# Kernel optimization log

Measured on AMD Instinct MI355X. Metric: run time of the kernel, lower is better.

## Reference

```python
import jax, jax.numpy as jnp
import numpy as np
import math

B, S, DIM = 2, 2048, 4096
N_HEADS, N_KV = 32, 8
HD = DIM // N_HEADS           # 128
N_REP = N_HEADS // N_KV       # 4
MAX_SEQ = 2048


def _rope_freqs(seq_len, head_dim):
    inv = 1.0 / (10000.0 ** (np.arange(0, head_dim, 2, dtype=np.float32) / head_dim))
    ang = np.outer(np.arange(seq_len, dtype=np.float32), inv)  # [S, HD/2]
    return jnp.asarray(np.cos(ang)), jnp.asarray(np.sin(ang))


def setup_inputs() -> dict:
    key = jax.random.key(0)
    ks = jax.random.split(key, 5)
    x = jax.random.normal(ks[0], (B, S, DIM), dtype=jnp.float32)
    wq = jax.random.normal(ks[1], (DIM, N_HEADS * HD), dtype=jnp.float32) * 0.02
    wk = jax.random.normal(ks[2], (DIM, N_KV * HD), dtype=jnp.float32) * 0.02
    wv = jax.random.normal(ks[3], (DIM, N_KV * HD), dtype=jnp.float32) * 0.02
    wo = jax.random.normal(ks[4], (N_HEADS * HD, DIM), dtype=jnp.float32) * 0.02
    freqs_cos, freqs_sin = _rope_freqs(S, HD)
    return {"x": x, "wq": wq, "wk": wk, "wv": wv, "wo": wo,
            "freqs_cos": freqs_cos, "freqs_sin": freqs_sin, "start_pos": 0}


def _apply_rope(t, cos, sin):
    # t: [B, S, H, HD]; adjacent pairs (2i, 2i+1) form complex numbers
    tr = t.reshape(*t.shape[:-1], HD // 2, 2)
    xr, xi = tr[..., 0], tr[..., 1]
    c = cos[None, :, None, :]  # [1, S, 1, HD/2]
    s = sin[None, :, None, :]
    o = jnp.stack([xr * c - xi * s, xr * s + xi * c], axis=-1)
    return o.reshape(t.shape)


def reference(x, wq, wk, wv, wo, freqs_cos, freqs_sin, start_pos):
    batch, seq_len, _ = x.shape
    q = (x @ wq).reshape(batch, seq_len, N_HEADS, HD)
    k = (x @ wk).reshape(batch, seq_len, N_KV, HD)
    v = (x @ wv).reshape(batch, seq_len, N_KV, HD)
    xq = _apply_rope(q, freqs_cos, freqs_sin)
    xk = _apply_rope(k, freqs_cos, freqs_sin)

    # KV-cache append (buffer initialized to zeros, as in the module)
    cache_k = jnp.zeros((batch, MAX_SEQ, N_KV, HD), dtype=x.dtype)
    cache_v = jnp.zeros((batch, MAX_SEQ, N_KV, HD), dtype=x.dtype)
    cache_k = jax.lax.dynamic_update_slice(cache_k, xk, (0, start_pos, 0, 0))
    cache_v = jax.lax.dynamic_update_slice(cache_v, v, (0, start_pos, 0, 0))
    keys = cache_k[:, : start_pos + seq_len]    # [B, T, KV, HD]
    values = cache_v[:, : start_pos + seq_len]

    # GQA: repeat kv heads n_rep times
    keys = jnp.repeat(keys, N_REP, axis=2)      # [B, T, H, HD]
    values = jnp.repeat(values, N_REP, axis=2)

    # [B, H, Sq, T] scores; no causal mask, matching the original module
    scores = jnp.einsum("bqhd,bkhd->bhqk", xq, keys) / math.sqrt(HD)
    attn = jax.nn.softmax(scores, axis=-1)
    out = jnp.einsum("bhqk,bkhd->bqhd", attn, values)
    out = out.reshape(batch, seq_len, N_HEADS * HD)
    return out @ wo
```

## Files before the change

kernel.cpp:

```cpp
#include <hip/hip_runtime.h>

#define S_LEN 2048

typedef __bf16 bf16x8 __attribute__((ext_vector_type(8)));
typedef float f32x4 __attribute__((ext_vector_type(4)));

static __device__ __forceinline__ unsigned short f32_to_bf16(float f){
  unsigned int u = __float_as_uint(f);
  u += 0x7FFFu + ((u >> 16) & 1u);
  return (unsigned short)(u >> 16);
}
static __device__ __forceinline__ float bf16_to_f32(unsigned short h){
  return __uint_as_float(((unsigned int)h) << 16);
}
static __device__ __forceinline__ bf16x8 ld_bf16x8(const unsigned short* p){
  return *reinterpret_cast<const bf16x8*>(p);
}
static __device__ __forceinline__ void async_copy16(const void* g, void* l){
  __builtin_amdgcn_global_load_lds(
      (const __attribute__((address_space(1))) void*)g,
      (__attribute__((address_space(3))) void*)l, 16, 0, 0);
}

#define MFMA16 __builtin_amdgcn_mfma_f32_16x16x32_bf16
#define GBAR()   asm volatile("s_barrier" ::: "memory")
#define LGKM0()  do { asm volatile("s_waitcnt lgkmcnt(0)" ::: "memory"); \
                      __builtin_amdgcn_sched_barrier(0); } while(0)
#define VMW(N)   asm volatile("s_waitcnt vmcnt(" #N ")" ::: "memory")

#define XCD_SWZ(bxv, byv) \
  int flat_ = blockIdx.y * gridDim.x + blockIdx.x; \
  const int cpx_ = (gridDim.x * gridDim.y) >> 3; \
  flat_ = (flat_ & 7) * cpx_ + (flat_ >> 3); \
  const int bxv = flat_ % gridDim.x; \
  const int byv = flat_ / gridDim.x;

__global__ void conv_f32_bf16(const float* __restrict__ in, unsigned short* __restrict__ out, int n4){
  int i = blockIdx.x * 256 + threadIdx.x;
  if (i >= n4) return;
  float4 v = ((const float4*)in)[i];
  ushort4 o;
  o.x = f32_to_bf16(v.x); o.y = f32_to_bf16(v.y);
  o.z = f32_to_bf16(v.z); o.w = f32_to_bf16(v.w);
  ((ushort4*)out)[i] = o;
}

__global__ void transpose_w(const float* __restrict__ in, unsigned short* __restrict__ out, int K, int N){
  __shared__ float tile[32][33];
  int n0 = blockIdx.x * 32, k0 = blockIdx.y * 32;
  int tx = threadIdx.x, ty = threadIdx.y;
  #pragma unroll
  for (int i=0;i<4;++i)
    tile[ty + i*8][tx] = in[(size_t)(k0 + ty + i*8) * N + n0 + tx];
  __syncthreads();
  #pragma unroll
  for (int i=0;i<4;++i)
    out[(size_t)(n0 + ty + i*8) * K + k0 + tx] = f32_to_bf16(tile[tx][ty + i*8]);
}

__global__ void transpose_v(const unsigned short* __restrict__ in, unsigned short* __restrict__ out){
  __shared__ unsigned short tile[32][33];
  int r0 = blockIdx.x * 32;
  int c0 = blockIdx.y * 32;
  int tx = threadIdx.x, ty = threadIdx.y;
  #pragma unroll
  for (int i=0;i<4;++i)
    tile[ty + i*8][tx] = in[(size_t)(r0 + ty + i*8) * 6144 + 5120 + c0 + tx];
  __syncthreads();
  #pragma unroll
  for (int i=0;i<4;++i)
    out[(size_t)(c0 + ty + i*8) * 4096 + r0 + tx] = tile[tx][ty + i*8];
}

__global__ void rope_inplace(unsigned short* __restrict__ t, const float* __restrict__ cs,
                             const float* __restrict__ sn, int heads, float scale){
  int idx = blockIdx.x * 256 + threadIdx.x;
  int j = idx & 63;
  int tmp = idx >> 6;
  int h = tmp & (heads - 1);
  int row = tmp / heads;
  int s = row & (S_LEN - 1);
  float c = cs[s*64 + j], si = sn[s*64 + j];
  size_t base = (size_t)row * 6144 + (h << 7) + (j << 1);
  unsigned int pr = *reinterpret_cast<const unsigned int*>(&t[base]);
  float xr = bf16_to_f32((unsigned short)(pr & 0xFFFFu));
  float xi = bf16_to_f32((unsigned short)(pr >> 16));
  unsigned int lo = f32_to_bf16((xr * c - xi * si) * scale);
  unsigned int hi = f32_to_bf16((xr * si + xi * c) * scale);
  *reinterpret_cast<unsigned int*>(&t[base]) = lo | (hi << 16);
}

#define STG(gp, lp) do { \
    async_copy16((gp),             (lp) + wofs); \
    async_copy16((gp) + (Ks<<6),   (lp) + 4096 + wofs); \
  } while(0)

static __device__ __forceinline__ void read_a4(bf16x8 (&a)[4][2], const unsigned short* base, int s0, int s1){
  #pragma unroll
  for (int m=0;m<4;++m){
    const unsigned short* p = base + m*1024;
    a[m][0] = ld_bf16x8(p + s0);
    a[m][1] = ld_bf16x8(p + s1);
  }
}
template<int NO>
static __device__ __forceinline__ void read_b2(bf16x8 (&b)[4][2], const unsigned short* base, int s0, int s1){
  #pragma unroll
  for (int n=0;n<2;++n){
    const unsigned short* p = base + (NO+n)*1024;
    b[NO+n][0] = ld_bf16x8(p + s0);
    b[NO+n][1] = ld_bf16x8(p + s1);
  }
}
template<int MO, int NO>
static __device__ __forceinline__ void mfma_quad(f32x4 (&acc)[8][4], const bf16x8 (&a)[4][2], const bf16x8 (&b)[4][2]){
  __builtin_amdgcn_s_setprio(1);
  #pragma unroll
  for (int ks=0; ks<2; ++ks)
    #pragma unroll
    for (int m=0;m<4;++m)
      #pragma unroll
      for (int n=0;n<2;++n)
        acc[MO+m][NO+n] = MFMA16(a[m][ks], b[NO+n][ks], acc[MO+m][NO+n], 0, 0, 0);
  __builtin_amdgcn_s_setprio(0);
}

template<bool OUT_BF16>
__global__ __launch_bounds__(512, 2) void gemm256_bt(
    const unsigned short* __restrict__ A,
    const unsigned short* __restrict__ Bt,
    void* __restrict__ Cout, int N, int K)
{
  __shared__ alignas(16) unsigned short sm[65536];
  unsigned short* A0 = sm;
  unsigned short* B0 = sm + 16384;
  unsigned short* A1 = sm + 32768;
  unsigned short* B1 = sm + 49152;

  const int tid  = threadIdx.x;
  const int wave = tid >> 6;
  const int lane = tid & 63;
  const int lm = lane & 15;
  const int kq = lane >> 4;
  const int wm = wave >> 2;
  const int wn = wave & 3;
  const int wofs = wave * 512;
  const int srow = wave * 8 + (lane >> 3);
  const int scol = ((lane & 7) ^ (lane >> 3)) * 8;
  const int s0 = (kq ^ (lm & 7)) * 8;
  const int s1 = s0 ^ 32;

  XCD_SWZ(bxx, byy);
  const size_t Ks = (size_t)K;
  const size_t bm = (size_t)byy * 256;
  const size_t bn = (size_t)bxx * 256;
  const unsigned short* Asrc = A  + (bm + srow) * Ks + scol;
  const unsigned short* Bsrc = Bt + (bn + srow) * Ks + scol;
  const size_t h1 = (size_t)128 * Ks;

  const int ardo = (wm*128 + lm) * 64;
  const int brdo = (wn*64  + lm) * 64;

  const f32x4 zero4 = {0.f,0.f,0.f,0.f};
  f32x4 acc[8][4];
  #pragma unroll
  for (int i=0;i<8;++i)
    #pragma unroll
    for (int j=0;j<4;++j) acc[i][j] = zero4;
  bf16x8 a[4][2], b[4][2];

  const int NT = K >> 6;

  STG(Bsrc,           B0);
  STG(Bsrc + h1,      B0 + 8192);
  STG(Asrc,           A0);
  STG(Asrc + h1,      A0 + 8192);
  STG(Bsrc + 64,      B1);
  STG(Bsrc + h1 + 64, B1 + 8192);
  VMW(4);
  GBAR();

  for (int it = 0; it < (NT >> 1); ++it){
    const int k1 = (2*it + 1) * 64;
    const int k2 = ((2*it + 2) & (NT - 1)) * 64;
    const int k3 = ((2*it + 3) & (NT - 1)) * 64;
    read_a4(a, A0 + ardo, s0, s1);
    read_b2<0>(b, B0 + brdo, s0, s1);
    STG(Asrc + k1, A1);
    GBAR(); LGKM0(); mfma_quad<0,0>(acc, a, b); GBAR();
    read_b2<2>(b, B0 + brdo, s0, s1);
    STG(Asrc + h1 + k1, A1 + 8192);
    GBAR(); LGKM0(); mfma_quad<0,2>(acc, a, b); GBAR();
    read_a4(a, A0 + ardo + 4096, s0, s1);
    STG(Bsrc + k2, B0);
    GBAR(); LGKM0(); mfma_quad<4,0>(acc, a, b); GBAR();
    STG(Bsrc + h1 + k2, B0 + 8192);
    VMW(4);
    GBAR(); LGKM0(); mfma_quad<4,2>(acc, a, b); GBAR();
    read_a4(a, A1 + ardo, s0, s1);
    read_b2<0>(b, B1 + brdo, s0, s1);
    STG(Asrc + k2, A0);
    GBAR(); LGKM0(); mfma_quad<0,0>(acc, a, b); GBAR();
    read_b2<2>(b, B1 + brdo, s0, s1);
    STG(Asrc + h1 + k2, A0 + 8192);
    GBAR(); LGKM0(); mfma_quad<0,2>(acc, a, b); GBAR();
    read_a4(a, A1 + ardo + 4096, s0, s1);
    STG(Bsrc + k3, B1);
    GBAR(); LGKM0(); mfma_quad<4,0>(acc, a, b); GBAR();
    STG(Bsrc + h1 + k3, B1 + 8192);
    VMW(4);
    GBAR(); LGKM0(); mfma_quad<4,2>(acc, a, b); GBAR();
  }
  VMW(0);

  #pragma unroll
  for (int mi=0; mi<8; ++mi){
    const size_t row = bm + wm*128 + mi*16 + kq*4;
    #pragma unroll
    for (int ni=0; ni<4; ++ni){
      const size_t col = bn + wn*64 + ni*16 + lm;
      #pragma unroll
      for (int r=0; r<4; ++r){
        if constexpr (OUT_BF16)
          ((unsigned short*)Cout)[(row + r) * N + col] = f32_to_bf16(acc[mi][ni][r]);
        else
          ((float*)Cout)[(row + r) * N + col] = acc[mi][ni][r];
      }
    }
  }
}

template<bool OUT_BF16>
__global__ __launch_bounds__(256, 2) void gemm128_bt(
    const unsigned short* __restrict__ A,
    const unsigned short* __restrict__ Bt,
    void* __restrict__ Cout, int N, int K)
{
  __shared__ alignas(16) unsigned short Asm[128 * 32];
  __shared__ alignas(16) unsigned short Bsm[128 * 32];
  const int tid  = threadIdx.x;
  const int wave = tid >> 6;
  const int lane = tid & 63;
  const int lm = lane & 15;
  const int kq = lane >> 4;
  const int wm = (wave >> 1) * 64;
  const int wn = (wave & 1) * 64;
  XCD_SWZ(bxx, byy);
  const size_t bm = (size_t)byy * 128;
  const size_t bn = (size_t)bxx * 128;

  const f32x4 zero4 = {0.f, 0.f, 0.f, 0.f};
  f32x4 acc[4][4];
  #pragma unroll
  for (int i=0;i<4;++i)
    #pragma unroll
    for (int j=0;j<4;++j) acc[i][j] = zero4;

  const int srow = lane >> 2;
  const int sc   = ((lane & 3) ^ ((lane >> 3) & 3)) * 8;
  const unsigned short* gA0 = A  + (bm + wave*32      + srow) * (size_t)K + sc;
  const unsigned short* gA1 = A  + (bm + wave*32 + 16 + srow) * (size_t)K + sc;
  const unsigned short* gB0 = Bt + (bn + wave*32      + srow) * (size_t)K + sc;
  const unsigned short* gB1 = Bt + (bn + wave*32 + 16 + srow) * (size_t)K + sc;
  unsigned short* lA0 = &Asm[(wave*32     ) * 32];
  unsigned short* lA1 = &Asm[(wave*32 + 16) * 32];
  unsigned short* lB0 = &Bsm[(wave*32     ) * 32];
  unsigned short* lB1 = &Bsm[(wave*32 + 16) * 32];

  const int p8 = (kq ^ ((lm >> 1) & 3)) * 8;

  for (int k0 = 0; k0 < K; k0 += 32){
    async_copy16(gA0, lA0);
    async_copy16(gA1, lA1);
    async_copy16(gB0, lB0);
    async_copy16(gB1, lB1);
    gA0 += 32; gA1 += 32; gB0 += 32; gB1 += 32;
    __syncthreads();

    bf16x8 af[4], bfr[4];
    #pragma unroll
    for (int i=0;i<4;++i){
      af[i]  = ld_bf16x8(&Asm[(wm + i*16 + lm)*32 + p8]);
      bfr[i] = ld_bf16x8(&Bsm[(wn + i*16 + lm)*32 + p8]);
    }
    #pragma unroll
    for (int mi=0; mi<4; ++mi)
      #pragma unroll
      for (int ni=0; ni<4; ++ni)
        acc[mi][ni] = MFMA16(af[mi], bfr[ni], acc[mi][ni], 0, 0, 0);
    __syncthreads();
  }

  #pragma unroll
  for (int mi=0; mi<4; ++mi){
    #pragma unroll
    for (int ni=0; ni<4; ++ni){
      #pragma unroll
      for (int r=0; r<4; ++r){
        size_t row = bm + wm + mi*16 + kq*4 + r;
        size_t col = bn + wn + ni*16 + lm;
        if constexpr (OUT_BF16)
          ((unsigned short*)Cout)[row * N + col] = f32_to_bf16(acc[mi][ni][r]);
        else
          ((float*)Cout)[row * N + col] = acc[mi][ni][r];
      }
    }
  }
}

#define PP 72
#define QKV_STRIDE 6144

__global__ __launch_bounds__(512, 1) void flash_attn(
    const unsigned short* __restrict__ QKV,
    const unsigned short* __restrict__ VT,
    unsigned short* __restrict__ O)
{
  __shared__ alignas(16) unsigned short Ksm[2][64 * 128];
  __shared__ alignas(16) unsigned short VTsm[2][128 * 64];
  __shared__ alignas(16) unsigned short Psm[8 * 32 * PP];

  const int tid  = threadIdx.x;
  const int wave = tid >> 6;
  const int lane = tid & 63;
  const int lm = lane & 15;
  const int kq = lane >> 4;
  const int b   = blockIdx.z;
  XCD_SWZ(qb, h);
  const int kvh = h >> 2;
  const int q0  = qb * 256;

  bf16x8 qf[2][4];
  #pragma unroll
  for (int mt=0; mt<2; ++mt){
    const size_t qbase = (size_t)(b * S_LEN + q0 + wave*32 + mt*16 + lm) * QKV_STRIDE + h * 128;
    #pragma unroll
    for (int kf=0; kf<4; ++kf)
      qf[mt][kf] = ld_bf16x8(&QKV[qbase + kf*32 + kq*8]);
  }

  const f32x4 zero4 = {0.f,0.f,0.f,0.f};
  f32x4 Oacc[2][8];
  #pragma unroll
  for (int mt=0; mt<2; ++mt)
    #pragma unroll
    for (int i=0;i<8;++i) Oacc[mt][i] = zero4;
  f32x4 lacc[2] = {zero4, zero4};

  union { unsigned short s[8]; bf16x8 v; } ou;
  #pragma unroll
  for (int i=0;i<8;++i) ou.s[i] = 0x3F80;
  const bf16x8 ones = ou.v;

  const unsigned short* Kg = QKV + 4096 + (size_t)kvh * 128 + (size_t)b * S_LEN * QKV_STRIDE;
  const unsigned short* Vg = VT + (size_t)kvh * 128 * 4096 + (size_t)b * S_LEN;
  unsigned short* Pw = &Psm[wave * 32 * PP];

  const int kkey_in = lane >> 4;
  const int kccp    = lane & 15;
  const int vd_in   = lane >> 3;
  const int vchl    = ((lane & 7) ^ (vd_in & 7)) * 8;

  auto stage = [&](int kt, int buf) {
    unsigned short* Kd = Ksm[buf];
    unsigned short* Vd = VTsm[buf];
    #pragma unroll
    for (int c=0;c<2;++c){
      int kb4 = (wave*2 + c) * 4;
      int key = kb4 + kkey_in;
      int ccl = kccp ^ (key & 7);
      async_copy16(Kg + (size_t)(kt*64 + key) * QKV_STRIDE + ccl*8, Kd + kb4*128);
    }
    #pragma unroll
    for (int c=0;c<2;++c){
      int d0 = (wave*2 + c) * 8;
      int d  = d0 + vd_in;
      async_copy16(Vg + (size_t)d * 4096 + kt*64 + vchl, Vd + d0*64);
    }
  };

  stage(0, 0);
  for (int kt = 0; kt < S_LEN/64; ++kt){
    const int cur = kt & 1;
    if (kt + 1 < S_LEN/64){
      stage(kt + 1, cur ^ 1);
      VMW(4);
    } else {
      VMW(0);
    }
    GBAR();
    const unsigned short* Kc = Ksm[cur];
    const unsigned short* Vc = VTsm[cur];

    f32x4 sacc[2][4];
    #pragma unroll
    for (int nt=0;nt<4;++nt){ sacc[0][nt] = zero4; sacc[1][nt] = zero4; }
    __builtin_amdgcn_s_setprio(1);
    #pragma unroll
    for (int nt=0; nt<4; ++nt){
      const int n = nt*16 + lm;
      #pragma unroll
      for (int kf=0; kf<4; ++kf){
        int pc = ((kf*4 + kq) ^ (lm & 7)) * 8;
        bf16x8 kfrag = ld_bf16x8(&Kc[n*128 + pc]);
        sacc[0][nt] = MFMA16(qf[0][kf], kfrag, sacc[0][nt], 0,0,0);
        sacc[1][nt] = MFMA16(qf[1][kf], kfrag, sacc[1][nt], 0,0,0);
      }
    }
    __builtin_amdgcn_s_setprio(0);

    #pragma unroll
    for (int mt=0; mt<2; ++mt){
      #pragma unroll
      for (int nt=0; nt<4; ++nt){
        #pragma unroll
        for (int e=0; e<4; ++e){
          float p = __expf(sacc[mt][nt][e]);
          Pw[(mt*16 + kq*4 + e)*PP + nt*16 + lm] = f32_to_bf16(p);
        }
      }
    }

    __builtin_amdgcn_s_setprio(1);
    #pragma unroll
    for (int kf2=0; kf2<2; ++kf2){
      bf16x8 pf0 = ld_bf16x8(&Pw[(     lm)*PP + kf2*32 + kq*8]);
      bf16x8 pf1 = ld_bf16x8(&Pw[(16 + lm)*PP + kf2*32 + kq*8]);
      lacc[0] = MFMA16(pf0, ones, lacc[0], 0,0,0);
      lacc[1] = MFMA16(pf1, ones, lacc[1], 0,0,0);
      #pragma unroll
      for (int dt=0; dt<8; ++dt){
        int pc = ((kf2*4 + kq) ^ (lm & 7)) * 8;
        bf16x8 vfr = ld_bf16x8(&Vc[(dt*16 + lm)*64 + pc]);
        Oacc[0][dt] = MFMA16(pf0, vfr, Oacc[0][dt], 0,0,0);
        Oacc[1][dt] = MFMA16(pf1, vfr, Oacc[1][dt], 0,0,0);
      }
    }
    __builtin_amdgcn_s_setprio(0);
    GBAR();
  }

  #pragma unroll
  for (int mt=0; mt<2; ++mt){
    float inv[4];
    #pragma unroll
    for (int r=0;r<4;++r) inv[r] = __builtin_amdgcn_rcpf(lacc[mt][r]);
    const size_t obase = (((size_t)(b * S_LEN + q0 + wave*32 + mt*16 + kq*4)) * 32 + h) * 128;
    #pragma unroll
    for (int r=0;r<4;++r){
      #pragma unroll
      for (int dt=0; dt<8; ++dt)
        O[obase + (size_t)r * 4096 + dt*16 + lm] = f32_to_bf16(Oacc[mt][dt][r] * inv[r]);
    }
  }
}

extern "C" void kernel_launch(void* const* d_in, const int* in_sizes, int n_in,
                              void* d_out, int out_size, void* d_ws, size_t ws_size,
                              hipStream_t stream)
{
  const float* x    = (const float*)d_in[0];
  const float* wq   = (const float*)d_in[1];
  const float* wk   = (const float*)d_in[2];
  const float* wv   = (const float*)d_in[3];
  const float* wo   = (const float*)d_in[4];
  const float* fcos = (const float*)d_in[5];
  const float* fsin = (const float*)d_in[6];

  float* out = (float*)d_out;
  char* w = (char*)d_ws;
  const size_t MB = 1ull << 20;
  unsigned short* xb    = (unsigned short*)(w + 0);
  unsigned short* wqkvT = (unsigned short*)(w + 32*MB);
  unsigned short* woT   = (unsigned short*)(w + 80*MB);
  unsigned short* qkv   = (unsigned short*)(w + 112*MB);
  unsigned short* vT    = (unsigned short*)(w + 32*MB);
  unsigned short* attn  = (unsigned short*)(w + 0);

  conv_f32_bf16<<<dim3(16384), dim3(256), 0, stream>>>(x, xb, 4194304);

  transpose_w<<<dim3(128,128), dim3(32,8), 0, stream>>>(wq, wqkvT,                      4096, 4096);
  transpose_w<<<dim3(32,128),  dim3(32,8), 0, stream>>>(wk, wqkvT + (size_t)4096*4096, 4096, 1024);
  transpose_w<<<dim3(32,128),  dim3(32,8), 0, stream>>>(wv, wqkvT + (size_t)5120*4096, 4096, 1024);
  transpose_w<<<dim3(128,128), dim3(32,8), 0, stream>>>(wo, woT, 4096, 4096);

  gemm256_bt<true><<<dim3(16,16), dim3(512), 0, stream>>>(xb, wqkvT, qkv, 6144, 4096);
  gemm128_bt<true><<<dim3(16,32), dim3(256), 0, stream>>>(
      xb, wqkvT + (size_t)4096*4096, qkv + 4096, 6144, 4096);

  rope_inplace<<<dim3(32768), dim3(256), 0, stream>>>(qkv,        fcos, fsin, 32, 0.08838834764831845f);
  rope_inplace<<<dim3(8192),  dim3(256), 0, stream>>>(qkv + 4096, fcos, fsin, 8, 1.0f);

  transpose_v<<<dim3(128,32), dim3(32,8), 0, stream>>>(qkv, vT);

  flash_attn<<<dim3(8, 32, 2), dim3(512), 0, stream>>>(qkv, vT, attn);

  gemm256_bt<false><<<dim3(16,16), dim3(512), 0, stream>>>(attn, woT, out, 4096, 4096);
}
```

Before: 748.6 us.

## Merge QKV GEMMs, deepen A-tile prefetch, and use exp2 with per-tile P in attention

The separate 128-tile K/V GEMM is removed, and the 256-tile GEMM now covers all 6144 QKV columns in one launch. In the GEMM main loop, A-tile global loads are issued one phase earlier and the wait count becomes 6, so more loads are in flight behind the MFMAs. In flash attention, the log2(e) factor is folded into the Q scale so exp2f can replace __expf. The P staging buffer is cut to one swizzled 16-row tile per wave and processed per m-tile, which shrinks LDS use and raises launch_bounds occupancy from 1 to 4. Each change targets a different cost: launch count, load latency, transcendental cost and occupancy. Together they risk register pressure and ordering hazards.

```diff
diff --git a/kernel.cpp b/kernel.cpp
--- a/kernel.cpp
+++ b/kernel.cpp
@@ -177,7 +177,8 @@
   STG(Asrc + h1,      A0 + 8192);
   STG(Bsrc + 64,      B1);
   STG(Bsrc + h1 + 64, B1 + 8192);
-  VMW(4);
+  STG(Asrc + 64,      A1);
+  VMW(6);
   GBAR();
 
   for (int it = 0; it < (NT >> 1); ++it){
@@ -186,29 +187,29 @@
     const int k3 = ((2*it + 3) & (NT - 1)) * 64;
     read_a4(a, A0 + ardo, s0, s1);
     read_b2<0>(b, B0 + brdo, s0, s1);
-    STG(Asrc + k1, A1);
+    STG(Asrc + h1 + k1, A1 + 8192);
     GBAR(); LGKM0(); mfma_quad<0,0>(acc, a, b); GBAR();
     read_b2<2>(b, B0 + brdo, s0, s1);
-    STG(Asrc + h1 + k1, A1 + 8192);
     GBAR(); LGKM0(); mfma_quad<0,2>(acc, a, b); GBAR();
     read_a4(a, A0 + ardo + 4096, s0, s1);
     STG(Bsrc + k2, B0);
     GBAR(); LGKM0(); mfma_quad<4,0>(acc, a, b); GBAR();
     STG(Bsrc + h1 + k2, B0 + 8192);
-    VMW(4);
+    STG(Asrc + k2, A0);
+    VMW(6);
     GBAR(); LGKM0(); mfma_quad<4,2>(acc, a, b); GBAR();
     read_a4(a, A1 + ardo, s0, s1);
     read_b2<0>(b, B1 + brdo, s0, s1);
-    STG(Asrc + k2, A0);
+    STG(Asrc + h1 + k2, A0 + 8192);
     GBAR(); LGKM0(); mfma_quad<0,0>(acc, a, b); GBAR();
     read_b2<2>(b, B1 + brdo, s0, s1);
-    STG(Asrc + h1 + k2, A0 + 8192);
     GBAR(); LGKM0(); mfma_quad<0,2>(acc, a, b); GBAR();
     read_a4(a, A1 + ardo + 4096, s0, s1);
     STG(Bsrc + k3, B1);
     GBAR(); LGKM0(); mfma_quad<4,0>(acc, a, b); GBAR();
     STG(Bsrc + h1 + k3, B1 + 8192);
-    VMW(4);
+    STG(Asrc + k3, A1);
+    VMW(6);
     GBAR(); LGKM0(); mfma_quad<4,2>(acc, a, b); GBAR();
   }
   VMW(0);
@@ -230,95 +231,16 @@
   }
 }
 
-template<bool OUT_BF16>
-__global__ __launch_bounds__(256, 2) void gemm128_bt(
-    const unsigned short* __restrict__ A,
-    const unsigned short* __restrict__ Bt,
-    void* __restrict__ Cout, int N, int K)
-{
-  __shared__ alignas(16) unsigned short Asm[128 * 32];
-  __shared__ alignas(16) unsigned short Bsm[128 * 32];
-  const int tid  = threadIdx.x;
-  const int wave = tid >> 6;
-  const int lane = tid & 63;
-  const int lm = lane & 15;
-  const int kq = lane >> 4;
-  const int wm = (wave >> 1) * 64;
-  const int wn = (wave & 1) * 64;
-  XCD_SWZ(bxx, byy);
-  const size_t bm = (size_t)byy * 128;
-  const size_t bn = (size_t)bxx * 128;
-
-  const f32x4 zero4 = {0.f, 0.f, 0.f, 0.f};
-  f32x4 acc[4][4];
-  #pragma unroll
-  for (int i=0;i<4;++i)
-    #pragma unroll
-    for (int j=0;j<4;++j) acc[i][j] = zero4;
-
-  const int srow = lane >> 2;
-  const int sc   = ((lane & 3) ^ ((lane >> 3) & 3)) * 8;
-  const unsigned short* gA0 = A  + (bm + wave*32      + srow) * (size_t)K + sc;
-  const unsigned short* gA1 = A  + (bm + wave*32 + 16 + srow) * (size_t)K + sc;
-  const unsigned short* gB0 = Bt + (bn + wave*32      + srow) * (size_t)K + sc;
-  const unsigned short* gB1 = Bt + (bn + wave*32 + 16 + srow) * (size_t)K + sc;
-  unsigned short* lA0 = &Asm[(wave*32     ) * 32];
-  unsigned short* lA1 = &Asm[(wave*32 + 16) * 32];
-  unsigned short* lB0 = &Bsm[(wave*32     ) * 32];
-  unsigned short* lB1 = &Bsm[(wave*32 + 16) * 32];
-
-  const int p8 = (kq ^ ((lm >> 1) & 3)) * 8;
-
-  for (int k0 = 0; k0 < K; k0 += 32){
-    async_copy16(gA0, lA0);
-    async_copy16(gA1, lA1);
-    async_copy16(gB0, lB0);
-    async_copy16(gB1, lB1);
-    gA0 += 32; gA1 += 32; gB0 += 32; gB1 += 32;
-    __syncthreads();
-
-    bf16x8 af[4], bfr[4];
-    #pragma unroll
-    for (int i=0;i<4;++i){
-      af[i]  = ld_bf16x8(&Asm[(wm + i*16 + lm)*32 + p8]);
-      bfr[i] = ld_bf16x8(&Bsm[(wn + i*16 + lm)*32 + p8]);
-    }
-    #pragma unroll
-    for (int mi=0; mi<4; ++mi)
-      #pragma unroll
-      for (int ni=0; ni<4; ++ni)
-        acc[mi][ni] = MFMA16(af[mi], bfr[ni], acc[mi][ni], 0, 0, 0);
-    __syncthreads();
-  }
-
-  #pragma unroll
-  for (int mi=0; mi<4; ++mi){
-    #pragma unroll
-    for (int ni=0; ni<4; ++ni){
-      #pragma unroll
-      for (int r=0; r<4; ++r){
-        size_t row = bm + wm + mi*16 + kq*4 + r;
-        size_t col = bn + wn + ni*16 + lm;
-        if constexpr (OUT_BF16)
-          ((unsigned short*)Cout)[row * N + col] = f32_to_bf16(acc[mi][ni][r]);
-        else
-          ((float*)Cout)[row * N + col] = acc[mi][ni][r];
-      }
-    }
-  }
-}
-
-#define PP 72
 #define QKV_STRIDE 6144
 
-__global__ __launch_bounds__(512, 1) void flash_attn(
+__global__ __launch_bounds__(512, 4) void flash_attn(
     const unsigned short* __restrict__ QKV,
     const unsigned short* __restrict__ VT,
     unsigned short* __restrict__ O)
 {
   __shared__ alignas(16) unsigned short Ksm[2][64 * 128];
   __shared__ alignas(16) unsigned short VTsm[2][128 * 64];
-  __shared__ alignas(16) unsigned short Psm[8 * 32 * PP];
+  __shared__ alignas(16) unsigned short Psm[8 * 16 * 64];
 
   const int tid  = threadIdx.x;
   const int wave = tid >> 6;
@@ -354,7 +276,7 @@
 
   const unsigned short* Kg = QKV + 4096 + (size_t)kvh * 128 + (size_t)b * S_LEN * QKV_STRIDE;
   const unsigned short* Vg = VT + (size_t)kvh * 128 * 4096 + (size_t)b * S_LEN;
-  unsigned short* Pw = &Psm[wave * 32 * PP];
+  unsigned short* Pw = &Psm[wave * 16 * 64];
 
   const int kkey_in = lane >> 4;
   const int kccp    = lane & 15;
@@ -415,28 +337,26 @@
       for (int nt=0; nt<4; ++nt){
         #pragma unroll
         for (int e=0; e<4; ++e){
-          float p = __expf(sacc[mt][nt][e]);
-          Pw[(mt*16 + kq*4 + e)*PP + nt*16 + lm] = f32_to_bf16(p);
+          float p = exp2f(sacc[mt][nt][e]);
+          int row = kq*4 + e;
+          int phys = (nt*2 + (lm >> 3)) ^ (row & 7);
+          Pw[row*64 + phys*8 + (lm & 7)] = f32_to_bf16(p);
         }
       }
-    }
-
-    __builtin_amdgcn_s_setprio(1);
-    #pragma unroll
-    for (int kf2=0; kf2<2; ++kf2){
-      bf16x8 pf0 = ld_bf16x8(&Pw[(     lm)*PP + kf2*32 + kq*8]);
-      bf16x8 pf1 = ld_bf16x8(&Pw[(16 + lm)*PP + kf2*32 + kq*8]);
-      lacc[0] = MFMA16(pf0, ones, lacc[0], 0,0,0);
-      lacc[1] = MFMA16(pf1, ones, lacc[1], 0,0,0);
-      #pragma unroll
-      for (int dt=0; dt<8; ++dt){
-        int pc = ((kf2*4 + kq) ^ (lm & 7)) * 8;
-        bf16x8 vfr = ld_bf16x8(&Vc[(dt*16 + lm)*64 + pc]);
-        Oacc[0][dt] = MFMA16(pf0, vfr, Oacc[0][dt], 0,0,0);
-        Oacc[1][dt] = MFMA16(pf1, vfr, Oacc[1][dt], 0,0,0);
+      __builtin_amdgcn_s_setprio(1);
+      #pragma unroll
+      for (int kf2=0; kf2<2; ++kf2){
+        bf16x8 pf = ld_bf16x8(&Pw[lm*64 + ((kf2*4 + kq) ^ (lm & 7))*8]);
+        lacc[mt] = MFMA16(pf, ones, lacc[mt], 0,0,0);
+        #pragma unroll
+        for (int dt=0; dt<8; ++dt){
+          int pc = ((kf2*4 + kq) ^ (lm & 7)) * 8;
+          bf16x8 vfr = ld_bf16x8(&Vc[(dt*16 + lm)*64 + pc]);
+          Oacc[mt][dt] = MFMA16(pf, vfr, Oacc[mt][dt], 0,0,0);
+        }
       }
-    }
-    __builtin_amdgcn_s_setprio(0);
+      __builtin_amdgcn_s_setprio(0);
+    }
     GBAR();
   }
 
@@ -484,11 +404,9 @@
   transpose_w<<<dim3(32,128),  dim3(32,8), 0, stream>>>(wv, wqkvT + (size_t)5120*4096, 4096, 1024);
   transpose_w<<<dim3(128,128), dim3(32,8), 0, stream>>>(wo, woT, 4096, 4096);
 
-  gemm256_bt<true><<<dim3(16,16), dim3(512), 0, stream>>>(xb, wqkvT, qkv, 6144, 4096);
-  gemm128_bt<true><<<dim3(16,32), dim3(256), 0, stream>>>(
-      xb, wqkvT + (size_t)4096*4096, qkv + 4096, 6144, 4096);
-
-  rope_inplace<<<dim3(32768), dim3(256), 0, stream>>>(qkv,        fcos, fsin, 32, 0.08838834764831845f);
+  gemm256_bt<true><<<dim3(24,16), dim3(512), 0, stream>>>(xb, wqkvT, qkv, 6144, 4096);
+
+  rope_inplace<<<dim3(32768), dim3(256), 0, stream>>>(qkv,        fcos, fsin, 32, 0.12751743f);
   rope_inplace<<<dim3(8192),  dim3(256), 0, stream>>>(qkv + 4096, fcos, fsin, 8, 1.0f);
 
   transpose_v<<<dim3(128,32), dim3(32,8), 0, stream>>>(qkv, vT);
```

Measured after the change: 1.125 ms. 50.2% more time.
